# Kernel tuning notes

Hardware: AMD Instinct MI355X
Metric: run time of the kernel (lower is better)

## Reference

```python
import jax, jax.numpy as jnp
import numpy as np

B, N, D = 32, 2048, 1024


def setup_inputs() -> dict:
    key = jax.random.key(0)
    k1, k2, k3, k4, k5, k6 = jax.random.split(key, 6)
    encoded = jax.random.normal(k1, (B, N, D), dtype=jnp.float32)
    decoder_state = jax.random.normal(k2, (B, D), dtype=jnp.float32)
    mask = jax.random.randint(k3, (B, N), 0, 2, dtype=jnp.int32)
    scale = 1.0 / np.sqrt(D)
    W1 = jax.random.normal(k4, (D, D), dtype=jnp.float32) * scale  # applied as x @ W1
    W2 = jax.random.normal(k5, (D, D), dtype=jnp.float32) * scale
    vt = jax.random.normal(k6, (D,), dtype=jnp.float32) * scale
    return {"encoded": encoded, "decoder_state": decoder_state, "mask": mask,
            "W1": W1, "W2": W2, "vt": vt}


def reference(encoded, decoder_state, mask, W1, W2, vt):
    temperature = 1.0
    # process_encoded: W1(encoded)  [B, N, D]
    enc = jnp.einsum('bnd,de->bne', encoded, W1)
    # W2(decoder_state)  [B, D] -> broadcast-add over N
    dec = decoder_state @ W2
    # vt(tanh(.)).squeeze(2)  -> logits [B, N]
    u = jnp.einsum('bnd,d->bn', jnp.tanh(enc + dec[:, None, :]), vt)
    # masked log-softmax with temperature over dim=1
    logits = u / temperature + jnp.log(mask.astype(u.dtype) + 1e-45)
    return jax.nn.log_softmax(logits, axis=1)
```

## Files before the change

kernel.cpp:

```cpp
#include <hip/hip_runtime.h>

typedef _Float16 half8 __attribute__((ext_vector_type(8)));
typedef _Float16 half4 __attribute__((ext_vector_type(4)));
typedef __fp16   pk2   __attribute__((ext_vector_type(2)));
typedef float    f32x4 __attribute__((ext_vector_type(4)));

#define GLOBAL_AS __attribute__((address_space(1)))
#define LDS_AS    __attribute__((address_space(3)))

static constexpr int Bb = 32;
static constexpr int Nn = 2048;
static constexpr int Dd = 1024;
static constexpr int M  = Bb * Nn;


__global__ void prep_w1(const float* __restrict__ W1, _Float16* __restrict__ W1TT) {
    int g = blockIdx.x * 256 + threadIdx.x;
    int chunk = g >> 10;
    int u = g & 1023;
    int q = u >> 7, sc = u & 127;
    int cl = sc ^ (2 * (q & 3));
    int et = chunk >> 5, t = (chunk >> 1) & 15, h = chunk & 1;
    int e  = et * 256 + h * 128 + cl;
    int k0 = t * 64 + q * 8;
    half8 hh;
#pragma unroll
    for (int j = 0; j < 8; ++j)
        hh[j] = (_Float16)W1[(size_t)(k0 + j) * Dd + e];
    *(half8*)(W1TT + (size_t)g * 8) = hh;
}

__global__ void prep_enc(const float* __restrict__ A, _Float16* __restrict__ A_p) {
    __shared__ _Float16 T[128 * 64];
    const int c = blockIdx.x;
    const int tid = threadIdx.x;
    const int mtile = c >> 5, t = (c >> 1) & 15, h = c & 1;
    const int r0 = tid >> 4, ks = tid & 15;
    const int q = ks >> 1, h4 = ks & 1;
    const float* src0 = A + (size_t)(mtile * 256 + h * 128 + r0) * Dd
                          + t * 64 + ks * 4;
#pragma unroll
    for (int p = 0; p < 8; ++p) {
        const int r = p * 16 + r0;
        f32x4 a = *(const f32x4*)(src0 + (size_t)p * 16 * Dd);
        pk2 p0 = __builtin_amdgcn_cvt_pkrtz(a.x, a.y);
        pk2 p1 = __builtin_amdgcn_cvt_pkrtz(a.z, a.w);
        half4 hh; hh[0] = p0[0]; hh[1] = p0[1]; hh[2] = p1[0]; hh[3] = p1[1];
        *(half4*)(T + r * 64 + ((q ^ (r & 7)) * 8) + h4 * 4) = hh;
    }
    __syncthreads();
    const size_t cb = (size_t)c * 8192;
#pragma unroll
    for (int i = 0; i < 4; ++i) {
        int u = i * 256 + tid;
        int qq2 = u >> 7, sr = u & 127;
        int lr = sr ^ (2 * (qq2 & 3));
        half8 hh = *(const half8*)(T + lr * 64 + ((qq2 ^ (lr & 7)) * 8));
        *(half8*)(A_p + cb + (size_t)u * 8) = hh;
    }
}

__global__ void dec_kernel(const float* __restrict__ ds, const float* __restrict__ W2,
                           float* __restrict__ dec) {
    __shared__ float part[4][64];
    int b = blockIdx.x, ech = blockIdx.y;
    int tid = threadIdx.x;
    int e = ech * 64 + (tid & 63);
    int dc = tid >> 6;
    float acc = 0.f;
#pragma unroll 4
    for (int d = dc * 256; d < dc * 256 + 256; ++d)
        acc += ds[b * Dd + d] * W2[(size_t)d * Dd + e];
    part[dc][tid & 63] = acc;
    __syncthreads();
    if (tid < 64)
        dec[b * Dd + e] = part[0][tid] + part[1][tid] + part[2][tid] + part[3][tid];
}

#define BAR     asm volatile("s_barrier" ::: "memory")
#define LGKM(n) asm volatile("s_waitcnt lgkmcnt(" #n ")" ::: "memory")
#define VM(n)   asm volatile("s_waitcnt vmcnt(" #n ")" ::: "memory")
#define PRIO1   __builtin_amdgcn_s_setprio(1)
#define PRIO0   __builtin_amdgcn_s_setprio(0)

#define RD_A(dst, base) do { _Pragma("unroll") \
  for (int ks = 0; ks < 2; ++ks) { const int qb = ((ks * 4 + qq) * 128) * 8; \
    _Pragma("unroll") for (int m2 = 0; m2 < 4; ++m2) \
      dst[m2][ks] = *(const half8*)&lds[(base) + qb + (m2 * 32 + rA) * 8]; } } while (0)

#define RD_B(dst, base) do { _Pragma("unroll") \
  for (int ks = 0; ks < 2; ++ks) { const int qb = ((ks * 4 + qq) * 128) * 8; \
    _Pragma("unroll") for (int j2 = 0; j2 < 2; ++j2) \
      dst[j2][ks] = *(const half8*)&lds[(base) + qb + (j2 * 64 + rB) * 8]; } } while (0)

#define MFMAQ(A_, B_, ro, co) do { \
  _Pragma("unroll") for (int m2 = 0; m2 < 4; ++m2) \
  _Pragma("unroll") for (int j2 = 0; j2 < 2; ++j2) { \
    acc[(ro) + m2][(co) + j2] = __builtin_amdgcn_mfma_f32_16x16x32_f16( \
        A_[m2][0], B_[j2][0], acc[(ro) + m2][(co) + j2], 0, 0, 0); \
    acc[(ro) + m2][(co) + j2] = __builtin_amdgcn_mfma_f32_16x16x32_f16( \
        A_[m2][1], B_[j2][1], acc[(ro) + m2][(co) + j2], 0, 0, 0); } } while (0)

__global__ __launch_bounds__(512) void gemm8(
    const _Float16* __restrict__ A_p, const _Float16* __restrict__ W1TT,
    const float* __restrict__ dec, const float* __restrict__ vt,
    float* __restrict__ u_part)
{
    extern __shared__ _Float16 lds[];

    const int g  = blockIdx.x;
    const int wg = (g & 7) * 128 + (g >> 3);
    const int et    = wg & 3;
    const int mtile = wg >> 2;

    const int tid  = threadIdx.x;
    const int lane = tid & 63, wid = tid >> 6;
    const int wr = wid >> 2, wc = wid & 3;
    const int qq = lane >> 4, l15 = lane & 15;
    const int l15s = l15 ^ (2 * qq);
    const int rA = wr * 16 + l15s;
    const int rB = wc * 16 + l15s;

    f32x4 acc[8][4] = {};
    half8 ax[4][2], ay[4][2], b0[2][2], b1[2][2];

    const size_t abase = (size_t)mtile * 32 * 8192;
    const size_t bbase = (size_t)et * 32 * 8192;
    const int uoff = tid * 8;

    auto stA = [&](int T, int h) {
        const _Float16* gp = A_p + abase + ((size_t)(T * 2 + h) << 13) + uoff;
        _Float16* lp = lds + ((((T & 1) * 2 + h) << 13) + (wid << 9));
        __builtin_amdgcn_global_load_lds((const GLOBAL_AS void*)gp,
                                         (LDS_AS void*)lp, 16, 0, 0);
        __builtin_amdgcn_global_load_lds((const GLOBAL_AS void*)(gp + 4096),
                                         (LDS_AS void*)(lp + 4096), 16, 0, 0);
    };
    auto stB = [&](int T, int h) {
        const _Float16* gp = W1TT + bbase + ((size_t)(T * 2 + h) << 13) + uoff;
        _Float16* lp = lds + (32768 + (((T & 1) * 2 + h) << 13) + (wid << 9));
        __builtin_amdgcn_global_load_lds((const GLOBAL_AS void*)gp,
                                         (LDS_AS void*)lp, 16, 0, 0);
        __builtin_amdgcn_global_load_lds((const GLOBAL_AS void*)(gp + 4096),
                                         (LDS_AS void*)(lp + 4096), 16, 0, 0);
    };


    stA(0, 0); stA(0, 1); stB(0, 0); stB(0, 1);
    VM(0);
    BAR;

#pragma unroll 2
    for (int T = 0; T < 16; ++T) {
        const int As  = (T & 1) << 14;
        const int Bs2 = 32768 + ((T & 1) << 14);
        const bool s = (T < 15);

        if (s) { stA(T + 1, 0); stA(T + 1, 1); stB(T + 1, 0); stB(T + 1, 1); }

        RD_A(ax, As);
        RD_B(b0, Bs2);
        RD_B(b1, Bs2 + 8192);
        RD_A(ay, As + 8192);

        LGKM(12);
        PRIO1; MFMAQ(ax, b0, 0, 0); PRIO0;
        LGKM(8);
        PRIO1; MFMAQ(ax, b1, 0, 2); PRIO0;
        LGKM(0);
        PRIO1; MFMAQ(ay, b0, 4, 0); MFMAQ(ay, b1, 4, 2); PRIO0;

        VM(0);
        BAR;
    }

    const int b = mtile >> 3;
    float vtv[4], dcv[4];
#pragma unroll
    for (int nf = 0; nf < 4; ++nf) {
        int e = et * 256 + (nf >> 1) * 128 + (nf & 1) * 64 + wc * 16 + l15;
        vtv[nf] = vt[e];
        dcv[nf] = dec[b * Dd + e];
    }
    float* usum = (float*)lds;
#pragma unroll
    for (int hm = 0; hm < 8; ++hm) {
        const int h = hm >> 2, mq = hm & 3;
#pragma unroll
        for (int r = 0; r < 4; ++r) {
            float sv = 0.f;
#pragma unroll
            for (int nf = 0; nf < 4; ++nf) {
                float x  = acc[hm][nf][r] + dcv[nf];
                float ex = __expf(2.f * x);
                sv += (1.f - 2.f * __builtin_amdgcn_rcpf(ex + 1.f)) * vtv[nf];
            }
#pragma unroll
            for (int off = 1; off < 16; off <<= 1) sv += __shfl_xor(sv, off, 16);
            if (l15 == 0)
                usum[wc * 256 + h * 128 + mq * 32 + wr * 16 + qq * 4 + r] = sv;
        }
    }
    __syncthreads();
    if (tid < 256) {
        float v = usum[tid] + usum[256 + tid] + usum[512 + tid] + usum[768 + tid];
        u_part[(size_t)et * M + (size_t)mtile * 256 + tid] = v;
    }
}

__global__ void softmax_k(const float* __restrict__ up, const int* __restrict__ mask,
                          float* __restrict__ out) {
    __shared__ float red[8];
    int b = blockIdx.x, tid = threadIdx.x;
    float l[8];
#pragma unroll
    for (int i = 0; i < 8; ++i) {
        int n = i * 256 + tid;
        float s = up[(size_t)b * Nn + n];
#pragma unroll
        for (int et = 1; et < 4; ++et) s += up[(size_t)et * M + (size_t)b * Nn + n];
        l[i] = s + (mask[b * Nn + n] ? 0.f : -103.278931f);
    }
    float m = l[0];
#pragma unroll
    for (int i = 1; i < 8; ++i) m = fmaxf(m, l[i]);
#pragma unroll
    for (int o = 32; o >= 1; o >>= 1) m = fmaxf(m, __shfl_xor(m, o, 64));
    if ((tid & 63) == 0) red[tid >> 6] = m;
    __syncthreads();
    m = fmaxf(fmaxf(red[0], red[1]), fmaxf(red[2], red[3]));
    float s = 0.f;
#pragma unroll
    for (int i = 0; i < 8; ++i) s += expf(l[i] - m);
#pragma unroll
    for (int o = 32; o >= 1; o >>= 1) s += __shfl_xor(s, o, 64);
    if ((tid & 63) == 0) red[4 + (tid >> 6)] = s;
    __syncthreads();
    float lse = m + logf(red[4] + red[5] + red[6] + red[7]);
#pragma unroll
    for (int i = 0; i < 8; ++i)
        out[(size_t)b * Nn + i * 256 + tid] = l[i] - lse;
}

extern "C" void kernel_launch(void* const* d_in, const int* in_sizes, int n_in,
                              void* d_out, int out_size, void* d_ws, size_t ws_size,
                              hipStream_t stream) {
    const float* encoded = (const float*)d_in[0];
    const float* dstate  = (const float*)d_in[1];
    const int*   mask    = (const int*)d_in[2];
    const float* W1      = (const float*)d_in[3];
    const float* W2      = (const float*)d_in[4];
    const float* vt      = (const float*)d_in[5];
    float* out = (float*)d_out;

    char* ws = (char*)d_ws;
    float*    u_part = (float*)ws;
    float*    dec    = (float*)(ws + (size_t)4 * M * 4);
    _Float16* W1TT   = (_Float16*)(ws + (size_t)4 * M * 4 + (size_t)Bb * Dd * 4);
    _Float16* A_p    = (_Float16*)(ws + (size_t)4 * M * 4 + (size_t)Bb * Dd * 4
                                   + (size_t)Dd * Dd * 2);

    static bool attr_done = false;
    if (!attr_done) {
        hipFuncSetAttribute(reinterpret_cast<const void*>(gemm8),
                            hipFuncAttributeMaxDynamicSharedMemorySize, 131072);
        attr_done = true;
    }

    prep_w1<<<512, 256, 0, stream>>>(W1, W1TT);
    dec_kernel<<<dim3(32, 16), 256, 0, stream>>>(dstate, W2, dec);
    prep_enc<<<8192, 256, 0, stream>>>(encoded, A_p);
    gemm8<<<1024, 512, 131072, stream>>>(A_p, W1TT, dec, vt, u_part);
    softmax_k<<<32, 256, 0, stream>>>(u_part, mask, out);
}
```

Measured before the change: 554.5 us.

## Fuse fp32-to-fp16 encoded conversion into GEMM A-tile staging

Removes the separate prep_enc pass that converted and re-laid-out the fp32 encoded tensor into an fp16 workspace. The GEMM now loads fp32 A tiles into registers, converts them to fp16, and writes them swizzled into LDS, while B still uses direct global-to-LDS loads. This drops a full write and reread of a 128MB fp16 copy, at the cost of more register pressure and VALU/LDS-store work inside the main loop. A fragments are now reloaded into one register set, which reduces the overlap between LDS reads and MFMAs.

Measured after the change: 524.6 us. -5.4%, faster.

```diff
diff --git a/kernel.cpp b/kernel.cpp
--- a/kernel.cpp
+++ b/kernel.cpp
@@ -28,36 +28,6 @@
     for (int j = 0; j < 8; ++j)
         hh[j] = (_Float16)W1[(size_t)(k0 + j) * Dd + e];
     *(half8*)(W1TT + (size_t)g * 8) = hh;
-}
-
-__global__ void prep_enc(const float* __restrict__ A, _Float16* __restrict__ A_p) {
-    __shared__ _Float16 T[128 * 64];
-    const int c = blockIdx.x;
-    const int tid = threadIdx.x;
-    const int mtile = c >> 5, t = (c >> 1) & 15, h = c & 1;
-    const int r0 = tid >> 4, ks = tid & 15;
-    const int q = ks >> 1, h4 = ks & 1;
-    const float* src0 = A + (size_t)(mtile * 256 + h * 128 + r0) * Dd
-                          + t * 64 + ks * 4;
-#pragma unroll
-    for (int p = 0; p < 8; ++p) {
-        const int r = p * 16 + r0;
-        f32x4 a = *(const f32x4*)(src0 + (size_t)p * 16 * Dd);
-        pk2 p0 = __builtin_amdgcn_cvt_pkrtz(a.x, a.y);
-        pk2 p1 = __builtin_amdgcn_cvt_pkrtz(a.z, a.w);
-        half4 hh; hh[0] = p0[0]; hh[1] = p0[1]; hh[2] = p1[0]; hh[3] = p1[1];
-        *(half4*)(T + r * 64 + ((q ^ (r & 7)) * 8) + h4 * 4) = hh;
-    }
-    __syncthreads();
-    const size_t cb = (size_t)c * 8192;
-#pragma unroll
-    for (int i = 0; i < 4; ++i) {
-        int u = i * 256 + tid;
-        int qq2 = u >> 7, sr = u & 127;
-        int lr = sr ^ (2 * (qq2 & 3));
-        half8 hh = *(const half8*)(T + lr * 64 + ((qq2 ^ (lr & 7)) * 8));
-        *(half8*)(A_p + cb + (size_t)u * 8) = hh;
-    }
 }
 
 __global__ void dec_kernel(const float* __restrict__ ds, const float* __restrict__ W2,
@@ -102,7 +72,7 @@
         A_[m2][1], B_[j2][1], acc[(ro) + m2][(co) + j2], 0, 0, 0); } } while (0)
 
 __global__ __launch_bounds__(512) void gemm8(
-    const _Float16* __restrict__ A_p, const _Float16* __restrict__ W1TT,
+    const float* __restrict__ encA, const _Float16* __restrict__ W1TT,
     const float* __restrict__ dec, const float* __restrict__ vt,
     float* __restrict__ u_part)
 {
@@ -122,19 +92,35 @@
     const int rB = wc * 16 + l15s;
 
     f32x4 acc[8][4] = {};
-    half8 ax[4][2], ay[4][2], b0[2][2], b1[2][2];
-
-    const size_t abase = (size_t)mtile * 32 * 8192;
+    half8 a[4][2], b0[2][2], b1[2][2];
+    f32x4 aSt[8];
+
+    const int arow0 = tid >> 4;
+    const int l16   = tid & 15;
+    const int qw    = l16 >> 1, kh2 = l16 & 1;
+    const float* agp = encA + (((size_t)(mtile * 256 + arow0)) << 10) + l16 * 4;
+
     const size_t bbase = (size_t)et * 32 * 8192;
     const int uoff = tid * 8;
 
-    auto stA = [&](int T, int h) {
-        const _Float16* gp = A_p + abase + ((size_t)(T * 2 + h) << 13) + uoff;
-        _Float16* lp = lds + ((((T & 1) * 2 + h) << 13) + (wid << 9));
-        __builtin_amdgcn_global_load_lds((const GLOBAL_AS void*)gp,
-                                         (LDS_AS void*)lp, 16, 0, 0);
-        __builtin_amdgcn_global_load_lds((const GLOBAL_AS void*)(gp + 4096),
-                                         (LDS_AS void*)(lp + 4096), 16, 0, 0);
+    auto issueA = [&](int T) {
+        const float* gp = agp + T * 64;
+#pragma unroll
+        for (int p = 0; p < 8; ++p)
+            aSt[p] = *(const f32x4*)(gp + ((size_t)p << 15));
+    };
+    auto writeA = [&](int Tn) {
+        const int base = (Tn & 1) << 14;
+#pragma unroll
+        for (int p = 0; p < 8; ++p) {
+            const int r  = p * 32 + arow0;
+            const int h  = r >> 7, lr = r & 127;
+            const int lr2 = lr ^ (2 * (qw & 3));
+            pk2 c0 = __builtin_amdgcn_cvt_pkrtz(aSt[p][0], aSt[p][1]);
+            pk2 c1 = __builtin_amdgcn_cvt_pkrtz(aSt[p][2], aSt[p][3]);
+            half4 hh; hh[0] = c0[0]; hh[1] = c0[1]; hh[2] = c1[0]; hh[3] = c1[1];
+            *(half4*)&lds[base + h * 8192 + (qw * 128 + lr2) * 8 + kh2 * 4] = hh;
+        }
     };
     auto stB = [&](int T, int h) {
         const _Float16* gp = W1TT + bbase + ((size_t)(T * 2 + h) << 13) + uoff;
@@ -146,8 +132,10 @@
     };
 
 
-    stA(0, 0); stA(0, 1); stB(0, 0); stB(0, 1);
-    VM(0);
+    issueA(0); stB(0, 0); stB(0, 1);
+    VM(4);
+    writeA(0);
+    VM(0); LGKM(0);
     BAR;
 
 #pragma unroll 2
@@ -156,21 +144,21 @@
         const int Bs2 = 32768 + ((T & 1) << 14);
         const bool s = (T < 15);
 
-        if (s) { stA(T + 1, 0); stA(T + 1, 1); stB(T + 1, 0); stB(T + 1, 1); }
-
-        RD_A(ax, As);
+        if (s) { issueA(T + 1); stB(T + 1, 0); stB(T + 1, 1); }
+
+        RD_A(a, As);
         RD_B(b0, Bs2);
         RD_B(b1, Bs2 + 8192);
-        RD_A(ay, As + 8192);
-
-        LGKM(12);
-        PRIO1; MFMAQ(ax, b0, 0, 0); PRIO0;
-        LGKM(8);
-        PRIO1; MFMAQ(ax, b1, 0, 2); PRIO0;
+        LGKM(4);
+        PRIO1; MFMAQ(a, b0, 0, 0); PRIO0;
         LGKM(0);
-        PRIO1; MFMAQ(ay, b0, 4, 0); MFMAQ(ay, b1, 4, 2); PRIO0;
-
-        VM(0);
+        PRIO1; MFMAQ(a, b1, 0, 2); PRIO0;
+        RD_A(a, As + 8192);
+        LGKM(0);
+        PRIO1; MFMAQ(a, b0, 4, 0); MFMAQ(a, b1, 4, 2); PRIO0;
+
+        if (s) { VM(4); writeA(T + 1); }
+        VM(0); LGKM(0);
         BAR;
     }
 
@@ -257,8 +245,6 @@
     float*    u_part = (float*)ws;
     float*    dec    = (float*)(ws + (size_t)4 * M * 4);
     _Float16* W1TT   = (_Float16*)(ws + (size_t)4 * M * 4 + (size_t)Bb * Dd * 4);
-    _Float16* A_p    = (_Float16*)(ws + (size_t)4 * M * 4 + (size_t)Bb * Dd * 4
-                                   + (size_t)Dd * Dd * 2);
 
     static bool attr_done = false;
     if (!attr_done) {
@@ -269,7 +255,6 @@
 
     prep_w1<<<512, 256, 0, stream>>>(W1, W1TT);
     dec_kernel<<<dim3(32, 16), 256, 0, stream>>>(dstate, W2, dec);
-    prep_enc<<<8192, 256, 0, stream>>>(encoded, A_p);
-    gemm8<<<1024, 512, 131072, stream>>>(A_p, W1TT, dec, vt, u_part);
+    gemm8<<<1024, 512, 131072, stream>>>(encoded, W1TT, dec, vt, u_part);
     softmax_k<<<32, 256, 0, stream>>>(u_part, mask, out);
 }
```
